# Kernel tuning notes

Measured on AMD Instinct MI355X. Metric: run time of the kernel, lower is better.

Reference implementation:

```python
import jax, jax.numpy as jnp
import numpy as np

B, L, D_MODEL = 2, 4096, 1024
D_STATE, D_CONV, EXPAND, HEADDIM = 128, 4, 2, 64
D_INNER = EXPAND * D_MODEL              # 2048
NHEADS = D_INNER // HEADDIM             # 32
CONV_DIM = D_INNER + 2 * D_STATE        # 2304 (ngroups=1)
D_IN_PROJ = 2 * D_INNER + 2 * D_STATE + NHEADS  # 4384
CHUNK = 128
EPS = 1e-5


def _segsum(a):
    # a: (..., T) log-decays -> (..., T, T) lower-triangular segment sums, -inf above diagonal
    T = a.shape[-1]
    cs = jnp.cumsum(a, axis=-1)
    seg = cs[..., :, None] - cs[..., None, :]
    mask = jnp.tril(jnp.ones((T, T), dtype=bool))
    return jnp.where(mask, seg, -jnp.inf)


def _forward(x, norm_w, norm_b, in_proj_w, conv_w, conv_b, dt_bias, A_log, D, rms_w, out_proj_w):
    b, l, _ = x.shape
    # pre-LayerNorm
    mu = jnp.mean(x, -1, keepdims=True)
    var = jnp.mean(jnp.square(x - mu), -1, keepdims=True)
    xn = (x - mu) * jax.lax.rsqrt(var + EPS) * norm_w + norm_b
    zxbcdt = xn @ in_proj_w.T                              # (b,l,D_IN_PROJ)
    z = zxbcdt[..., :D_INNER]
    xBC = zxbcdt[..., D_INNER:D_INNER + CONV_DIM]
    dt = jax.nn.softplus(zxbcdt[..., -NHEADS:] + dt_bias)  # (b,l,h)
    # causal depthwise conv1d + SiLU over (x, B, C)
    xc = jnp.pad(xBC.transpose(0, 2, 1), ((0, 0), (0, 0), (D_CONV - 1, 0)))
    xc = jax.lax.conv_general_dilated(xc, conv_w[:, None, :], (1,), 'VALID',
                                      feature_group_count=CONV_DIM,
                                      dimension_numbers=('NCH', 'OIH', 'NCH'))
    xBC = jax.nn.silu(xc + conv_b[None, :, None]).transpose(0, 2, 1)
    xs = xBC[..., :D_INNER].reshape(b, l, NHEADS, HEADDIM)
    Bm = xBC[..., D_INNER:D_INNER + D_STATE]               # (b,l,n)
    Cm = xBC[..., D_INNER + D_STATE:]                      # (b,l,n)
    # SSD chunked selective scan
    A = -jnp.exp(A_log)                                    # (h,)
    a = dt * A                                             # (b,l,h) log decay
    X = xs * dt[..., None]                                 # (b,l,h,p)
    c = l // CHUNK
    a_c = a.reshape(b, c, CHUNK, NHEADS).transpose(0, 3, 1, 2)   # (b,h,c,s)
    a_cum = jnp.cumsum(a_c, -1)
    Lmat = jnp.exp(_segsum(a_c))                           # (b,h,c,s,s)
    Xc = X.reshape(b, c, CHUNK, NHEADS, HEADDIM)
    Bc = Bm.reshape(b, c, CHUNK, D_STATE)
    Cc = Cm.reshape(b, c, CHUNK, D_STATE)
    # intra-chunk (diagonal block) output
    Y_diag = jnp.einsum('bcln,bcsn,bhcls,bcshp->bclhp', Cc, Bc, Lmat, Xc)
    # chunk-final states
    decay_states = jnp.exp(a_cum[..., -1:] - a_cum)        # (b,h,c,s)
    states = jnp.einsum('bcln,bhcl,bclhp->bchpn', Bc, decay_states, Xc)
    states = jnp.concatenate([jnp.zeros_like(states[:, :1]), states], axis=1)
    chunk_decay = jnp.exp(_segsum(jnp.pad(a_cum[..., -1], ((0, 0), (0, 0), (1, 0)))))  # (b,h,c+1,c+1)
    prev = jnp.einsum('bhzc,bchpn->bzhpn', chunk_decay, states)[:, :-1]  # (b,c,h,p,n)
    # inter-chunk (off-diagonal) output
    Y_off = jnp.einsum('bcln,bchpn,bhcl->bclhp', Cc, prev, jnp.exp(a_cum))
    y = (Y_diag + Y_off).reshape(b, l, NHEADS, HEADDIM) + D[None, None, :, None] * xs
    y = y.reshape(b, l, D_INNER)
    # gated RMSNorm (norm_before_gate=False): norm(y * silu(z))
    y = y * jax.nn.silu(z)
    y = y * jax.lax.rsqrt(jnp.mean(jnp.square(y), -1, keepdims=True) + EPS) * rms_w
    return x + y @ out_proj_w.T


def setup_inputs() -> dict:
    key = jax.random.key(0)
    ks = jax.random.split(key, 8)
    return {
        'x': jax.random.normal(ks[0], (B, L, D_MODEL), jnp.float32),
        'norm_w': jnp.ones((D_MODEL,), jnp.float32),
        'norm_b': jnp.zeros((D_MODEL,), jnp.float32),
        'in_proj_w': 0.02 * jax.random.normal(ks[1], (D_IN_PROJ, D_MODEL), jnp.float32),
        'conv_w': 0.2 * jax.random.normal(ks[2], (CONV_DIM, D_CONV), jnp.float32),
        'conv_b': jnp.zeros((CONV_DIM,), jnp.float32),
        'dt_bias': jax.random.uniform(ks[3], (NHEADS,), jnp.float32, -4.0, 0.0),
        'A_log': jnp.log(jax.random.uniform(ks[4], (NHEADS,), jnp.float32, 1.0, 16.0)),
        'D': jnp.ones((NHEADS,), jnp.float32),
        'rms_w': jnp.ones((D_INNER,), jnp.float32),
        'out_proj_w': 0.02 * jax.random.normal(ks[5], (D_MODEL, D_INNER), jnp.float32),
    }


def reference(x, norm_w, norm_b, in_proj_w, conv_w, conv_b, dt_bias, A_log, D, rms_w, out_proj_w):
    return _forward(x, norm_w, norm_b, in_proj_w, conv_w, conv_b, dt_bias, A_log, D, rms_w, out_proj_w)
```

## Files before the change

### kernel.cpp

```cpp
#include <hip/hip_runtime.h>

#define B_ 2
#define L_ 4096
#define DMODEL 1024
#define DSTATE 128
#define DINNER 2048
#define NH 32
#define HD 64
#define DPROJ 4384
#define DPROJP 4480
#define NC 32
#define EPSF 1e-5f
#define ROWS (B_*L_)

typedef unsigned short u16;
typedef __attribute__((ext_vector_type(8))) short s8v;
typedef __attribute__((ext_vector_type(4))) float f4v;
typedef __attribute__((ext_vector_type(4))) int i4v;
typedef __attribute__((ext_vector_type(2))) int i2v;
typedef __attribute__((ext_vector_type(4))) float fl4;

static __device__ __forceinline__ float b2f(u16 u){
  unsigned int x = ((unsigned int)u) << 16;
  return __builtin_bit_cast(float, x);
}
static __device__ __forceinline__ u16 f2b(float f){
  unsigned int x = __builtin_bit_cast(unsigned int, f);
  unsigned int r = x + 0x7FFFu + ((x >> 16) & 1u);
  return (u16)(r >> 16);
}
static __device__ __forceinline__ float softplusf(float x){
  return (x > 20.f) ? x : log1pf(expf(x));
}
static __device__ __forceinline__ void gl_lds16(const u16* g, u16* l){
  __builtin_amdgcn_global_load_lds(
    (const __attribute__((address_space(1))) unsigned int*)g,
    (__attribute__((address_space(3))) unsigned int*)l, 16, 0, 0);
}
static __device__ __forceinline__ int swz(int row, int col){
  return row*128 + ((((col >> 3) ^ (row & 15)) << 3) | (col & 7));
}
static __device__ __forceinline__ int swz64(int row, int col){
  return row*64 + ((((col >> 3) ^ (row & 7)) << 3) | (col & 7));
}
static __device__ __forceinline__ int osw(int t, int j){
  return t*64 + ((((j >> 3) ^ ((t >> 3) & 7)) << 3) | (j & 7));
}

__global__ void k_dbg(float* out, float v){ out[0] = v; }

__global__ __launch_bounds__(256) void k_pack_w1(const float* __restrict__ W, u16* __restrict__ Wb){
  size_t i = (size_t)blockIdx.x*256 + threadIdx.x;
  if (i >= (size_t)DPROJP*DMODEL) return;
  size_t n = i / DMODEL;
  Wb[i] = (n < DPROJ) ? f2b(W[i]) : (u16)0;
}
__global__ __launch_bounds__(256) void k_pack_w2(const float* __restrict__ W, u16* __restrict__ Wb){
  size_t i = (size_t)blockIdx.x*256 + threadIdx.x;
  if (i >= (size_t)DMODEL*DINNER) return;
  Wb[i] = f2b(W[i]);
}

__global__ __launch_bounds__(256) void k_ln(const float* __restrict__ x, const float* __restrict__ nw,
                                            const float* __restrict__ nb, u16* __restrict__ xn){
  int m = blockIdx.x; int tid = threadIdx.x;
  const float* row = x + (size_t)m*DMODEL;
  fl4 v = *(const fl4*)&row[tid*4];
  float s1 = v[0]+v[1]+v[2]+v[3];
  float s2 = v[0]*v[0]+v[1]*v[1]+v[2]*v[2]+v[3]*v[3];
  #pragma unroll
  for (int o=32;o;o>>=1){ s1 += __shfl_down(s1,o); s2 += __shfl_down(s2,o); }
  __shared__ float r1[4], r2[4];
  if ((tid&63)==0){ r1[tid>>6]=s1; r2[tid>>6]=s2; }
  __syncthreads();
  s1 = r1[0]+r1[1]+r1[2]+r1[3]; s2 = r2[0]+r2[1]+r2[2]+r2[3];
  float mu = s1 * (1.f/DMODEL);
  float var = s2 * (1.f/DMODEL) - mu*mu;
  float rs = rsqrtf(var + EPSF);
  u16* o = xn + (size_t)m*DMODEL + tid*4;
  #pragma unroll
  for (int k=0;k<4;k++)
    o[k] = f2b((v[k]-mu)*rs*nw[tid*4+k] + nb[tid*4+k]);
}

template<int MODE>
__global__ __launch_bounds__(256) void k_gemm(const u16* __restrict__ A, const u16* __restrict__ Bw,
                  void* __restrict__ Cout, const float* __restrict__ resid,
                  int K, int lda, int ldb, int ldc){
  __shared__ u16 smem[2*128*64];
  u16* sA = smem;
  u16* sB = smem + 128*64;
  int tid = threadIdx.x;
  int ln = tid & 63, wid = tid >> 6;
  int wr = wid >> 1, wc = wid & 1;
  size_t m0 = (size_t)blockIdx.x * 128, n0 = (size_t)blockIdx.y * 128;
  int lrow = ln >> 3;
  f4v acc[4][4] = {};
  for (int k0 = 0; k0 < K; k0 += 64){
    #pragma unroll
    for (int i = 0; i < 4; ++i){
      int seg = wid*4 + i;
      int row = seg*8 + lrow;
      int scol = ((ln & 7) ^ (row & 7)) * 8;
      gl_lds16(&A [(m0+row)*lda + k0 + scol], &sA[seg*512]);
      gl_lds16(&Bw[(n0+row)*ldb + k0 + scol], &sB[seg*512]);
    }
    __syncthreads();
    #pragma unroll
    for (int kk=0; kk<2; kk++){
      s8v af[4], bfr[4];
      #pragma unroll
      for (int t=0;t<4;t++){
        int col = kk*32 + (ln>>4)*8;
        af[t]  = *(const s8v*)&sA[swz64(wr*64+t*16+(ln&15), col)];
        bfr[t] = *(const s8v*)&sB[swz64(wc*64+t*16+(ln&15), col)];
      }
      #pragma unroll
      for (int mt=0;mt<4;mt++)
        #pragma unroll
        for (int nt=0;nt<4;nt++)
          acc[mt][nt] = __builtin_amdgcn_mfma_f32_16x16x32_bf16(af[mt], bfr[nt], acc[mt][nt], 0,0,0);
    }
    __syncthreads();
  }
  if (MODE == 0){
    #pragma unroll
    for (int mt=0;mt<4;mt++)
      #pragma unroll
      for (int nt=0;nt<4;nt++)
        #pragma unroll
        for (int j=0;j<4;j++){
          int m = wr*64 + mt*16 + (ln>>4)*4 + j;
          int n = wc*64 + nt*16 + (ln&15);
          smem[m*128 + n] = f2b(acc[mt][nt][j]);
        }
    __syncthreads();
    #pragma unroll
    for (int it = 0; it < 8; ++it){
      int idx = (tid + it*256)*8;
      int row = idx >> 7, col = idx & 127;
      *(i4v*)&((u16*)Cout)[(m0+row)*ldc + n0 + col] = *(const i4v*)&smem[idx];
    }
  } else {
    #pragma unroll
    for (int mt=0;mt<4;mt++)
      #pragma unroll
      for (int nt=0;nt<4;nt++)
        #pragma unroll
        for (int j=0;j<4;j++){
          size_t m = m0 + wr*64 + mt*16 + (ln>>4)*4 + j;
          size_t n = n0 + wc*64 + nt*16 + (ln&15);
          ((float*)Cout)[m*ldc + n] = acc[mt][nt][j] + resid[m*ldc + n];
        }
  }
}

__global__ __launch_bounds__(256) void k_conv(const u16* __restrict__ zx, const float* __restrict__ cw,
    const float* __restrict__ cb, const float* __restrict__ dtb, const float* __restrict__ Dp,
    u16* __restrict__ Y, u16* __restrict__ Xt, u16* __restrict__ Bln, u16* __restrict__ Bt,
    u16* __restrict__ Cln, float* __restrict__ dtg){
  __shared__ u16 in_s[131*64];
  __shared__ u16 out_s[128*64];
  __shared__ float dt_s[128];
  int bid = blockIdx.x;
  int g = bid % 36;
  int c = (bid / 36) & 31;
  int b = bid / (36*32);
  int tid = threadIdx.x;
  int t0 = c*128;
  size_t rowb = (size_t)b*L_ + t0;
  for (int i8 = tid; i8 < 1048; i8 += 256){
    int r = i8 >> 3, j0 = (i8 & 7)*8;
    int t = t0 - 3 + r;
    i4v v;
    if (t >= 0) v = *(const i4v*)&zx[((size_t)b*L_ + t)*DPROJP + 2048 + g*64 + j0];
    else { v[0]=0; v[1]=0; v[2]=0; v[3]=0; }
    *(i4v*)&in_s[r*64 + j0] = v;
  }
  if (g < 32 && tid < 128){
    float raw = b2f(zx[(rowb + tid)*DPROJP + (DPROJ - NH) + g]);
    float d = softplusf(raw + dtb[g]);
    dt_s[tid] = d;
    dtg[(rowb + tid)*NH + g] = d;
  }
  __syncthreads();
  {
    int j = tid & 63;
    int ch = g*64 + j;
    float w0 = cw[ch*4+0], w1 = cw[ch*4+1], w2 = cw[ch*4+2], w3 = cw[ch*4+3];
    float bia = cb[ch];
    int tb = tid >> 6;
    #pragma unroll
    for (int it = 0; it < 32; ++it){
      int t = tb + it*4;
      float a = bia
        + w0*b2f(in_s[(t+0)*64 + j]) + w1*b2f(in_s[(t+1)*64 + j])
        + w2*b2f(in_s[(t+2)*64 + j]) + w3*b2f(in_s[(t+3)*64 + j]);
      out_s[osw(t, j)] = f2b(a / (1.f + __expf(-a)));
    }
  }
  __syncthreads();
  if (g < 32){
    float Dh = Dp[g];
    for (int i = tid; i < 1024; i += 256){
      int t = i >> 3, j0 = (i & 7)*8;
      i4v v = *(const i4v*)&out_s[osw(t, j0)];
      const u16* vu = (const u16*)&v;
      i4v o; u16* ou = (u16*)&o;
      #pragma unroll
      for (int k = 0; k < 8; ++k) ou[k] = f2b(b2f(vu[k]) * Dh);
      *(i4v*)&Y[(rowb + t)*DINNER + g*64 + j0] = o;
    }
    for (int i = tid; i < 1024; i += 256){
      int j = i >> 4, tb = (i & 15)*8;
      i4v o; u16* ou = (u16*)&o;
      #pragma unroll
      for (int k = 0; k < 8; ++k)
        ou[k] = f2b(b2f(out_s[osw(tb + k, j)]) * dt_s[tb + k]);
      *(i4v*)&Xt[((size_t)((b*NH + g)*HD + j))*L_ + t0 + tb] = o;
    }
  } else {
    int q = g - 32;
    for (int i = tid; i < 1024; i += 256){
      int t = i >> 3, j0 = (i & 7)*8;
      i4v v = *(const i4v*)&out_s[osw(t, j0)];
      if (q < 2) *(i4v*)&Bln[(rowb + t)*DSTATE + q*64 + j0] = v;
      else       *(i4v*)&Cln[(rowb + t)*DSTATE + (q-2)*64 + j0] = v;
    }
    if (q < 2){
      for (int i = tid; i < 1024; i += 256){
        int j = i >> 4, tb = (i & 15)*8;
        i4v o; u16* ou = (u16*)&o;
        #pragma unroll
        for (int k = 0; k < 8; ++k) ou[k] = out_s[osw(tb + k, j)];
        *(i4v*)&Bt[((size_t)(b*DSTATE + q*64 + j))*L_ + t0 + tb] = o;
      }
    }
  }
}

__global__ __launch_bounds__(128) void k_acum(const float* __restrict__ dtg, const float* __restrict__ A_log,
                                              float* __restrict__ acum){
  int bid = blockIdx.x;
  int c = bid & 31, h = (bid >> 5) & 31, b = bid >> 10;
  int l = threadIdx.x;
  __shared__ float a[128];
  float Ah = -expf(A_log[h]);
  a[l] = dtg[((size_t)(b*L_ + c*128 + l))*NH + h] * Ah;
  __syncthreads();
  #pragma unroll
  for (int d = 1; d < 128; d <<= 1){
    float v = (l >= d) ? a[l-d] : 0.f;
    __syncthreads();
    a[l] += v;
    __syncthreads();
  }
  acum[(size_t)bid*128 + l] = a[l];
}

__global__ __launch_bounds__(256) void k_states(const u16* __restrict__ Xt, const u16* __restrict__ Bt,
    const float* __restrict__ acum, u16* __restrict__ states){
  __shared__ u16 sX[64*128];
  __shared__ u16 sB[128*128];
  __shared__ float dec[128];
  int bid = blockIdx.x;
  int h = bid & 31, c = (bid >> 5) & 31, b = bid >> 10;
  int tid = threadIdx.x;
  const float* acg = acum + ((size_t)((b*NH + h)*NC + c))*128;
  if (tid < 128) dec[tid] = __expf(acg[127] - acg[tid]);
  __syncthreads();
  const u16* xtb = Xt + ((size_t)((b*NH + h)*HD))*L_ + c*128;
  for (int i = tid*8; i < 64*128; i += 256*8){
    int p = i >> 7, l0 = i & 127;
    i4v v = *(const i4v*)&xtb[(size_t)p*L_ + l0];
    const u16* vu = (const u16*)&v;
    i4v o; u16* ou = (u16*)&o;
    #pragma unroll
    for (int j = 0; j < 8; ++j) ou[j] = f2b(b2f(vu[j]) * dec[l0 + j]);
    *(i4v*)&sX[swz(p, l0)] = o;
  }
  const u16* btb = Bt + (size_t)(b*DSTATE)*L_ + c*128;
  for (int i = tid*8; i < 128*128; i += 256*8){
    int n = i >> 7, l0 = i & 127;
    *(i4v*)&sB[swz(n, l0)] = *(const i4v*)&btb[(size_t)n*L_ + l0];
  }
  __syncthreads();
  int ln = tid & 63, wid = tid >> 6;
  int wr = wid >> 1, wc = wid & 1;
  f4v acc[2][4] = {};
  #pragma unroll
  for (int kk = 0; kk < 4; ++kk){
    s8v af[2], bfr[4];
    int col = kk*32 + (ln>>4)*8;
    #pragma unroll
    for (int t = 0; t < 2; ++t)
      af[t] = *(const s8v*)&sX[swz(wr*32 + t*16 + (ln&15), col)];
    #pragma unroll
    for (int t = 0; t < 4; ++t)
      bfr[t] = *(const s8v*)&sB[swz(wc*64 + t*16 + (ln&15), col)];
    #pragma unroll
    for (int mt = 0; mt < 2; ++mt)
      #pragma unroll
      for (int nt = 0; nt < 4; ++nt)
        acc[mt][nt] = __builtin_amdgcn_mfma_f32_16x16x32_bf16(af[mt], bfr[nt], acc[mt][nt], 0,0,0);
  }
  u16* out = states + ((size_t)((b*NC + c)*NH + h))*(HD*DSTATE);
  #pragma unroll
  for (int mt = 0; mt < 2; ++mt)
    #pragma unroll
    for (int nt = 0; nt < 4; ++nt){
      int n = wc*64 + nt*16 + (ln&15);
      #pragma unroll
      for (int j = 0; j < 4; ++j){
        int p = wr*32 + mt*16 + (ln>>4)*4 + j;
        out[(size_t)p*DSTATE + n] = f2b(acc[mt][nt][j]);
      }
    }
}

__global__ __launch_bounds__(256) void k_scan(u16* __restrict__ states, const float* __restrict__ acum){
  int bid = blockIdx.x;
  int eb = bid & 7;
  int hb = bid >> 3;
  int h = hb & 31, b = hb >> 5;
  int tid = threadIdx.x;
  float run[4] = {0.f, 0.f, 0.f, 0.f};
  size_t ebase = (size_t)eb*1024 + (size_t)tid*4;
  for (int c = 0; c < NC; ++c){
    float dec = __expf(acum[((size_t)((b*NH + h)*NC + c))*128 + 127]);
    u16* st = states + ((size_t)((b*NC + c)*NH + h))*(HD*DSTATE) + ebase;
    i2v w = *(const i2v*)st;
    const u16* wu = (const u16*)&w;
    i2v o; u16* ou = (u16*)&o;
    #pragma unroll
    for (int j = 0; j < 4; ++j){
      float tmp = b2f(wu[j]);
      float r = run[j];
      ou[j] = f2b(r);
      run[j] = r*dec + tmp;
    }
    *(i2v*)st = o;
  }
}

__global__ __launch_bounds__(256) void k_y(const u16* __restrict__ Cln, const u16* __restrict__ Bln,
    const u16* __restrict__ Xt, const u16* __restrict__ prev, const float* __restrict__ acum,
    u16* __restrict__ Y){
  __shared__ u16 sC[128*128];
  __shared__ u16 sBS[128*128];
  int bid = blockIdx.x;
  int h = bid & 31, c = (bid >> 5) & 31, b = bid >> 10;
  int tid = threadIdx.x;
  size_t rowb = (size_t)b*L_ + c*128;
  const float* acg = acum + ((size_t)((b*NH + h)*NC + c))*128;
  for (int i = tid*8; i < 128*128; i += 256*8){
    int row = i >> 7, col = i & 127;
    int d = swz(row, col);
    *(i4v*)&sC[d]  = *(const i4v*)&Cln[(rowb + row)*DSTATE + col];
    *(i4v*)&sBS[d] = *(const i4v*)&Bln[(rowb + row)*DSTATE + col];
  }
  __syncthreads();
  int ln = tid & 63, wid = tid >> 6;
  int wr = wid >> 1, wc = wid & 1;
  f4v aS[4][4] = {};
  #pragma unroll
  for (int kk = 0; kk < 4; ++kk){
    s8v af[4], bfr[4];
    #pragma unroll
    for (int t = 0; t < 4; ++t){
      int col = kk*32 + (ln>>4)*8;
      af[t]  = *(const s8v*)&sC [swz(wr*64 + t*16 + (ln&15), col)];
      bfr[t] = *(const s8v*)&sBS[swz(wc*64 + t*16 + (ln&15), col)];
    }
    #pragma unroll
    for (int mt = 0; mt < 4; ++mt)
      #pragma unroll
      for (int nt = 0; nt < 4; ++nt)
        aS[mt][nt] = __builtin_amdgcn_mfma_f32_16x16x32_bf16(af[mt], bfr[nt], aS[mt][nt], 0,0,0);
  }
  __syncthreads();
  #pragma unroll
  for (int mt = 0; mt < 4; ++mt)
    #pragma unroll
    for (int nt = 0; nt < 4; ++nt){
      int s = wc*64 + nt*16 + (ln&15);
      float as = acg[s];
      #pragma unroll
      for (int j = 0; j < 4; ++j){
        int l = wr*64 + mt*16 + (ln>>4)*4 + j;
        float v = (s <= l) ? aS[mt][nt][j] * __expf(acg[l] - as) : 0.f;
        sBS[swz(l, s)] = f2b(v);
      }
    }
  __syncthreads();
  const u16* xtb = Xt + ((size_t)((b*NH + h)*HD))*L_ + c*128;
  const u16* pv = prev + ((size_t)((b*NC + c)*NH + h))*(HD*DSTATE);
  f4v aD[4][2] = {}, aO[4][2] = {};
  #pragma unroll
  for (int kk = 0; kk < 4; ++kk){
    s8v aSf[4], aCf[4], bXf[2], bPf[2];
    #pragma unroll
    for (int t = 0; t < 4; ++t){
      int col = kk*32 + (ln>>4)*8;
      int row = wr*64 + t*16 + (ln&15);
      aSf[t] = *(const s8v*)&sBS[swz(row, col)];
      aCf[t] = *(const s8v*)&sC[swz(row, col)];
    }
    #pragma unroll
    for (int t = 0; t < 2; ++t){
      int p = wc*32 + t*16 + (ln&15);
      int ko = kk*32 + (ln>>4)*8;
      bXf[t] = *(const s8v*)&xtb[(size_t)p*L_ + ko];
      bPf[t] = *(const s8v*)&pv[(size_t)p*DSTATE + ko];
    }
    #pragma unroll
    for (int mt = 0; mt < 4; ++mt)
      #pragma unroll
      for (int nt = 0; nt < 2; ++nt){
        aD[mt][nt] = __builtin_amdgcn_mfma_f32_16x16x32_bf16(aSf[mt], bXf[nt], aD[mt][nt], 0,0,0);
        aO[mt][nt] = __builtin_amdgcn_mfma_f32_16x16x32_bf16(aCf[mt], bPf[nt], aO[mt][nt], 0,0,0);
      }
  }
  #pragma unroll
  for (int mt = 0; mt < 4; ++mt)
    #pragma unroll
    for (int nt = 0; nt < 2; ++nt){
      int p = wc*32 + nt*16 + (ln&15);
      #pragma unroll
      for (int j = 0; j < 4; ++j){
        int l = wr*64 + mt*16 + (ln>>4)*4 + j;
        float ex = __expf(acg[l]);
        size_t idx = (rowb + l)*DINNER + h*HD + p;
        float yv = aD[mt][nt][j] + ex*aO[mt][nt][j] + b2f(Y[idx]);
        Y[idx] = f2b(yv);
      }
    }
}

__global__ __launch_bounds__(256) void k_gate(u16* __restrict__ Y, const u16* __restrict__ zx,
                                              const float* __restrict__ rw){
  size_t m = blockIdx.x; int tid = threadIdx.x;
  u16* yrow = Y + m*DINNER + tid*8;
  const u16* zrow = zx + m*DPROJP + tid*8;
  i4v yv = *(const i4v*)yrow;
  i4v zv = *(const i4v*)zrow;
  const u16* yu = (const u16*)&yv;
  const u16* zu = (const u16*)&zv;
  float yg[8]; float ss = 0.f;
  #pragma unroll
  for (int k = 0; k < 8; ++k){
    float z = b2f(zu[k]);
    float g = z / (1.f + __expf(-z));
    float v = b2f(yu[k]) * g;
    yg[k] = v; ss += v*v;
  }
  #pragma unroll
  for (int o = 32; o; o >>= 1) ss += __shfl_down(ss, o);
  __shared__ float r[4];
  if ((tid&63) == 0) r[tid>>6] = ss;
  __syncthreads();
  ss = r[0]+r[1]+r[2]+r[3];
  float rstd = rsqrtf(ss*(1.f/DINNER) + EPSF);
  #pragma unroll
  for (int k = 0; k < 8; ++k)
    yrow[k] = f2b(yg[k]*rstd*rw[tid*8+k]);
}

extern "C" void kernel_launch(void* const* d_in, const int* in_sizes, int n_in,
                              void* d_out, int out_size, void* d_ws, size_t ws_size,
                              hipStream_t stream){
  const float* x        = (const float*)d_in[0];
  const float* norm_w   = (const float*)d_in[1];
  const float* norm_b   = (const float*)d_in[2];
  const float* in_proj  = (const float*)d_in[3];
  const float* conv_w   = (const float*)d_in[4];
  const float* conv_b   = (const float*)d_in[5];
  const float* dt_bias  = (const float*)d_in[6];
  const float* A_log    = (const float*)d_in[7];
  const float* Dp       = (const float*)d_in[8];
  const float* rms_w    = (const float*)d_in[9];
  const float* out_proj = (const float*)d_in[10];

  char* ws = (char*)d_ws;
  size_t off = 0;
  auto alloc = [&](size_t bytes) -> void* {
    void* p = ws + off;
    off += (bytes + 255) & ~(size_t)255;
    return p;
  };
  u16*   w1b    = (u16*)  alloc((size_t)DPROJP*DMODEL*2);
  u16*   w2b    = (u16*)  alloc((size_t)DMODEL*DINNER*2);
  u16*   xn     = (u16*)  alloc((size_t)ROWS*DMODEL*2);
  u16*   zx     = (u16*)  alloc((size_t)ROWS*DPROJP*2);
  u16*   Xt     = (u16*)  alloc((size_t)B_*NH*HD*L_*2);
  u16*   Bln    = (u16*)  alloc((size_t)ROWS*DSTATE*2);
  u16*   Bt     = (u16*)  alloc((size_t)B_*DSTATE*L_*2);
  u16*   Cln    = (u16*)  alloc((size_t)ROWS*DSTATE*2);
  float* dtg    = (float*)alloc((size_t)ROWS*NH*4);
  float* acum   = (float*)alloc((size_t)B_*NH*NC*128*4);
  u16*   Y      = (u16*)  alloc((size_t)ROWS*DINNER*2);
  u16* states = (u16*)d_out;
  if (off > ws_size){
    k_dbg<<<1, 1, 0, stream>>>((float*)d_out, (float)ws_size);
    return;
  }

  k_pack_w1<<<dim3((DPROJP*DMODEL + 255)/256), 256, 0, stream>>>(in_proj, w1b);
  k_pack_w2<<<dim3((DMODEL*DINNER + 255)/256), 256, 0, stream>>>(out_proj, w2b);
  k_ln<<<dim3(ROWS), 256, 0, stream>>>(x, norm_w, norm_b, xn);
  k_gemm<0><<<dim3(ROWS/128, DPROJP/128), 256, 0, stream>>>(xn, w1b, zx, nullptr,
                                                            DMODEL, DMODEL, DMODEL, DPROJP);
  k_conv<<<dim3(B_*NC*36), 256, 0, stream>>>(zx, conv_w, conv_b, dt_bias, Dp,
                                             Y, Xt, Bln, Bt, Cln, dtg);
  k_acum<<<dim3(B_*NH*NC), 128, 0, stream>>>(dtg, A_log, acum);
  k_states<<<dim3(B_*NC*NH), 256, 0, stream>>>(Xt, Bt, acum, states);
  k_scan<<<dim3(B_*NH*8), 256, 0, stream>>>(states, acum);
  k_y<<<dim3(B_*NC*NH), 256, 0, stream>>>(Cln, Bln, Xt, states, acum, Y);
  k_gate<<<dim3(ROWS), 256, 0, stream>>>(Y, zx, rms_w);
  k_gemm<1><<<dim3(ROWS/128, DMODEL/128), 256, 0, stream>>>(Y, w2b, d_out, x,
                                                            DINNER, DINNER, DINNER, DMODEL);
}
```

Measured before the change: 320.1 us.

## Fold D skip term into diagonal of intra-chunk matrix, stage Y writes via LDS

The D*x skip term is no longer written to Y by the conv kernel and read back in k_y. Instead it is added on the diagonal of the intra-chunk score matrix as D/dt, since Xt already carries the dt factor. k_y now stages its output tile in shared memory and writes Y with coalesced 16-byte stores instead of read-modify-write scalar accesses. The dt buffer is transposed to a head-major layout so k_acum and k_y read it contiguously, and k_scan preloads all chunk states and decays into registers before scanning. Dividing by dt adds bf16 rounding error on the diagonal, and the dt values could be small.

```diff
diff --git a/kernel.cpp b/kernel.cpp
--- a/kernel.cpp
+++ b/kernel.cpp
@@ -156,8 +156,8 @@
 }
 
 __global__ __launch_bounds__(256) void k_conv(const u16* __restrict__ zx, const float* __restrict__ cw,
-    const float* __restrict__ cb, const float* __restrict__ dtb, const float* __restrict__ Dp,
-    u16* __restrict__ Y, u16* __restrict__ Xt, u16* __restrict__ Bln, u16* __restrict__ Bt,
+    const float* __restrict__ cb, const float* __restrict__ dtb,
+    u16* __restrict__ Xt, u16* __restrict__ Bln, u16* __restrict__ Bt,
     u16* __restrict__ Cln, float* __restrict__ dtg){
   __shared__ u16 in_s[131*64];
   __shared__ u16 out_s[128*64];
@@ -181,7 +181,7 @@
     float raw = b2f(zx[(rowb + tid)*DPROJP + (DPROJ - NH) + g]);
     float d = softplusf(raw + dtb[g]);
     dt_s[tid] = d;
-    dtg[(rowb + tid)*NH + g] = d;
+    dtg[(size_t)(b*NH + g)*L_ + t0 + tid] = d;
   }
   __syncthreads();
   {
@@ -201,16 +201,6 @@
   }
   __syncthreads();
   if (g < 32){
-    float Dh = Dp[g];
-    for (int i = tid; i < 1024; i += 256){
-      int t = i >> 3, j0 = (i & 7)*8;
-      i4v v = *(const i4v*)&out_s[osw(t, j0)];
-      const u16* vu = (const u16*)&v;
-      i4v o; u16* ou = (u16*)&o;
-      #pragma unroll
-      for (int k = 0; k < 8; ++k) ou[k] = f2b(b2f(vu[k]) * Dh);
-      *(i4v*)&Y[(rowb + t)*DINNER + g*64 + j0] = o;
-    }
     for (int i = tid; i < 1024; i += 256){
       int j = i >> 4, tb = (i & 15)*8;
       i4v o; u16* ou = (u16*)&o;
@@ -246,7 +236,7 @@
   int l = threadIdx.x;
   __shared__ float a[128];
   float Ah = -expf(A_log[h]);
-  a[l] = dtg[((size_t)(b*L_ + c*128 + l))*NH + h] * Ah;
+  a[l] = dtg[(size_t)(b*NH + h)*L_ + c*128 + l] * Ah;
   __syncthreads();
   #pragma unroll
   for (int d = 1; d < 128; d <<= 1){
@@ -324,35 +314,44 @@
   int hb = bid >> 3;
   int h = hb & 31, b = hb >> 5;
   int tid = threadIdx.x;
+  size_t ebase = (size_t)eb*1024 + (size_t)tid*4;
+  size_t hoff = ((size_t)(b*NC*NH + h))*(HD*DSTATE) + ebase;
+  float dec[NC];
+  #pragma unroll
+  for (int c = 0; c < NC; ++c)
+    dec[c] = __expf(acum[((size_t)((b*NH + h)*NC + c))*128 + 127]);
+  i2v w[NC];
+  #pragma unroll
+  for (int c = 0; c < NC; ++c)
+    w[c] = *(const i2v*)&states[(size_t)c*(NH*HD*DSTATE) + hoff];
   float run[4] = {0.f, 0.f, 0.f, 0.f};
-  size_t ebase = (size_t)eb*1024 + (size_t)tid*4;
+  #pragma unroll
   for (int c = 0; c < NC; ++c){
-    float dec = __expf(acum[((size_t)((b*NH + h)*NC + c))*128 + 127]);
-    u16* st = states + ((size_t)((b*NC + c)*NH + h))*(HD*DSTATE) + ebase;
-    i2v w = *(const i2v*)st;
-    const u16* wu = (const u16*)&w;
-    i2v o; u16* ou = (u16*)&o;
+    u16* wu = (u16*)&w[c];
     #pragma unroll
     for (int j = 0; j < 4; ++j){
       float tmp = b2f(wu[j]);
-      float r = run[j];
-      ou[j] = f2b(r);
-      run[j] = r*dec + tmp;
-    }
-    *(i2v*)st = o;
-  }
+      wu[j] = f2b(run[j]);
+      run[j] = run[j]*dec[c] + tmp;
+    }
+  }
+  #pragma unroll
+  for (int c = 0; c < NC; ++c)
+    *(i2v*)&states[(size_t)c*(NH*HD*DSTATE) + hoff] = w[c];
 }
 
 __global__ __launch_bounds__(256) void k_y(const u16* __restrict__ Cln, const u16* __restrict__ Bln,
     const u16* __restrict__ Xt, const u16* __restrict__ prev, const float* __restrict__ acum,
-    u16* __restrict__ Y){
+    const float* __restrict__ dtg, const float* __restrict__ Dp, u16* __restrict__ Y){
   __shared__ u16 sC[128*128];
   __shared__ u16 sBS[128*128];
+  __shared__ float dt_s[128];
   int bid = blockIdx.x;
   int h = bid & 31, c = (bid >> 5) & 31, b = bid >> 10;
   int tid = threadIdx.x;
   size_t rowb = (size_t)b*L_ + c*128;
   const float* acg = acum + ((size_t)((b*NH + h)*NC + c))*128;
+  if (tid < 128) dt_s[tid] = dtg[(size_t)(b*NH + h)*L_ + c*128 + tid];
   for (int i = tid*8; i < 128*128; i += 256*8){
     int row = i >> 7, col = i & 127;
     int d = swz(row, col);
@@ -362,6 +361,7 @@
   __syncthreads();
   int ln = tid & 63, wid = tid >> 6;
   int wr = wid >> 1, wc = wid & 1;
+  float Dh = Dp[h];
   f4v aS[4][4] = {};
   #pragma unroll
   for (int kk = 0; kk < 4; ++kk){
@@ -388,7 +388,11 @@
       #pragma unroll
       for (int j = 0; j < 4; ++j){
         int l = wr*64 + mt*16 + (ln>>4)*4 + j;
-        float v = (s <= l) ? aS[mt][nt][j] * __expf(acg[l] - as) : 0.f;
+        float v = 0.f;
+        if (s <= l){
+          v = aS[mt][nt][j] * __expf(acg[l] - as);
+          if (s == l) v += Dh / dt_s[l];
+        }
         sBS[swz(l, s)] = f2b(v);
       }
     }
@@ -421,6 +425,7 @@
         aO[mt][nt] = __builtin_amdgcn_mfma_f32_16x16x32_bf16(aCf[mt], bPf[nt], aO[mt][nt], 0,0,0);
       }
   }
+  __syncthreads();
   #pragma unroll
   for (int mt = 0; mt < 4; ++mt)
     #pragma unroll
@@ -430,11 +435,18 @@
       for (int j = 0; j < 4; ++j){
         int l = wr*64 + mt*16 + (ln>>4)*4 + j;
         float ex = __expf(acg[l]);
-        size_t idx = (rowb + l)*DINNER + h*HD + p;
-        float yv = aD[mt][nt][j] + ex*aO[mt][nt][j] + b2f(Y[idx]);
-        Y[idx] = f2b(yv);
+        float yv = aD[mt][nt][j] + ex*aO[mt][nt][j];
+        sC[l*64 + (p ^ ((l & 7) << 3))] = f2b(yv);
       }
     }
+  __syncthreads();
+  #pragma unroll
+  for (int it = 0; it < 4; ++it){
+    int idx = (tid + it*256)*8;
+    int row = idx >> 6, col0 = idx & 63;
+    i4v v = *(const i4v*)&sC[row*64 + (col0 ^ ((row & 7) << 3))];
+    *(i4v*)&Y[(rowb + row)*DINNER + h*HD + col0] = v;
+  }
 }
 
 __global__ __launch_bounds__(256) void k_gate(u16* __restrict__ Y, const u16* __restrict__ zx,
@@ -496,7 +508,7 @@
   u16*   Bln    = (u16*)  alloc((size_t)ROWS*DSTATE*2);
   u16*   Bt     = (u16*)  alloc((size_t)B_*DSTATE*L_*2);
   u16*   Cln    = (u16*)  alloc((size_t)ROWS*DSTATE*2);
-  float* dtg    = (float*)alloc((size_t)ROWS*NH*4);
+  float* dtg    = (float*)alloc((size_t)B_*NH*L_*4);
   float* acum   = (float*)alloc((size_t)B_*NH*NC*128*4);
   u16*   Y      = (u16*)  alloc((size_t)ROWS*DINNER*2);
   u16* states = (u16*)d_out;
@@ -510,12 +522,12 @@
   k_ln<<<dim3(ROWS), 256, 0, stream>>>(x, norm_w, norm_b, xn);
   k_gemm<0><<<dim3(ROWS/128, DPROJP/128), 256, 0, stream>>>(xn, w1b, zx, nullptr,
                                                             DMODEL, DMODEL, DMODEL, DPROJP);
-  k_conv<<<dim3(B_*NC*36), 256, 0, stream>>>(zx, conv_w, conv_b, dt_bias, Dp,
-                                             Y, Xt, Bln, Bt, Cln, dtg);
+  k_conv<<<dim3(B_*NC*36), 256, 0, stream>>>(zx, conv_w, conv_b, dt_bias,
+                                             Xt, Bln, Bt, Cln, dtg);
   k_acum<<<dim3(B_*NH*NC), 128, 0, stream>>>(dtg, A_log, acum);
   k_states<<<dim3(B_*NC*NH), 256, 0, stream>>>(Xt, Bt, acum, states);
   k_scan<<<dim3(B_*NH*8), 256, 0, stream>>>(states, acum);
-  k_y<<<dim3(B_*NC*NH), 256, 0, stream>>>(Cln, Bln, Xt, states, acum, Y);
+  k_y<<<dim3(B_*NC*NH), 256, 0, stream>>>(Cln, Bln, Xt, states, acum, dtg, Dp, Y);
   k_gate<<<dim3(ROWS), 256, 0, stream>>>(Y, zx, rms_w);
   k_gemm<1><<<dim3(ROWS/128, DMODEL/128), 256, 0, stream>>>(Y, w2b, d_out, x,
                                                             DINNER, DINNER, DINNER, DMODEL);
```

Result: faster. 307.1 us (-4.1%).
